# Kernel optimization log

Hardware: AMD Instinct MI355X
Metric: run time of the kernel (lower is better)

Reference implementation:

```python
import jax, jax.numpy as jnp
from jax import lax
import numpy as np

B, T, U, V = 4, 300, 64, 1024
FEAT, H, L = 80, 512, 3            # encoder: 3-layer bidirectional LSTM
HD = 512                           # decoder hidden (1 layer)
ENC_OUT = DEC_OUT = 512
INNER = 512
DMAX = max(FEAT, 2 * H)            # padded input dim for stacked encoder weights
NEG = -1e30


def setup_inputs() -> dict:
    key = jax.random.key(0)
    ks = jax.random.split(key, 20)
    s = 1.0 / np.sqrt(H)
    u = lambda k, shp: jax.random.uniform(k, shp, jnp.float32, -s, s)
    inputs = jax.random.normal(ks[0], (B, T, FEAT), jnp.float32)
    inputs_length = jax.random.randint(ks[1], (B,), T // 2, T + 1, jnp.int32)
    targets = jax.random.randint(ks[2], (B, U), 1, V, jnp.int32)
    targets_length = jax.random.randint(ks[3], (B,), U // 2, U + 1, jnp.int32)
    enc_Wih = u(ks[4], (L, 2, 4 * H, DMAX))   # layer0 uses first FEAT cols
    enc_Whh = u(ks[5], (L, 2, 4 * H, H))
    enc_b = u(ks[6], (L, 2, 4 * H))           # b_ih + b_hh fused
    enc_proj_W = u(ks[7], (ENC_OUT, 2 * H))
    enc_proj_b = u(ks[8], (ENC_OUT,))
    dec_emb = u(ks[9], (V, HD)).at[0].set(0.0)  # padding_idx=0
    dec_Wih = u(ks[10], (4 * HD, HD))
    dec_Whh = u(ks[11], (4 * HD, HD))
    dec_b = u(ks[12], (4 * HD,))
    dec_proj_W = u(ks[13], (DEC_OUT, HD))
    dec_proj_b = u(ks[14], (DEC_OUT,))
    j_fwd_W = u(ks[15], (INNER, ENC_OUT + DEC_OUT))
    j_fwd_b = u(ks[16], (INNER,))
    j_proj_W = u(ks[17], (V, INNER))
    j_proj_b = u(ks[18], (V,))
    return dict(inputs=inputs, inputs_length=inputs_length, targets=targets,
                targets_length=targets_length, enc_Wih=enc_Wih, enc_Whh=enc_Whh,
                enc_b=enc_b, enc_proj_W=enc_proj_W, enc_proj_b=enc_proj_b,
                dec_emb=dec_emb, dec_Wih=dec_Wih, dec_Whh=dec_Whh, dec_b=dec_b,
                dec_proj_W=dec_proj_W, dec_proj_b=dec_proj_b, j_fwd_W=j_fwd_W,
                j_fwd_b=j_fwd_b, j_proj_W=j_proj_W, j_proj_b=j_proj_b)


def lstm_layer(x, Wih, Whh, b):
    # x: [B, T, Din]; torch gate order (i, f, g, o)
    Bb = x.shape[0]
    Hh = Whh.shape[1]
    xg = jnp.einsum('btd,gd->btg', x, Wih) + b  # precompute input projections

    def step(carry, xt):
        h, c = carry
        g = xt + h @ Whh.T
        i, f, gg, o = jnp.split(g, 4, axis=-1)
        c = jax.nn.sigmoid(f) * c + jax.nn.sigmoid(i) * jnp.tanh(gg)
        h = jax.nn.sigmoid(o) * jnp.tanh(c)
        return (h, c), h

    z = jnp.zeros((Bb, Hh), x.dtype)
    _, hs = lax.scan(step, (z, z), xg.transpose(1, 0, 2))
    return hs.transpose(1, 0, 2)


def reverse_padded(x, lengths):
    # reverse each sequence within its valid length (packed-sequence semantics)
    t = jnp.arange(x.shape[1])
    idx = jnp.where(t[None] < lengths[:, None], lengths[:, None] - 1 - t[None], t[None])
    return jnp.take_along_axis(x, idx[:, :, None], axis=1)


def rnnt_loss(log_probs, targets, T_len, U_len):
    # log_probs: [B, T, U+1, V], blank = 0
    Bb, Tt, U1, _ = log_probs.shape
    Uu = U1 - 1
    blank = log_probs[..., 0]                                   # [B,T,U+1]
    idx = jnp.broadcast_to(targets[:, None, :, None], (Bb, Tt, Uu, 1))
    lab = jnp.take_along_axis(log_probs[:, :, :Uu, :], idx, axis=3)[..., 0]  # [B,T,U]

    def row_update(a, c):
        # solves x[u] = logaddexp(a[u], x[u-1] + c[u-1]) via log-space cumsum
        C = jnp.concatenate([jnp.zeros((Bb, 1), a.dtype), jnp.cumsum(c, axis=1)], axis=1)
        return C + lax.cumlogsumexp(a - C, axis=1)

    a0 = jnp.full((Bb, U1), NEG, log_probs.dtype).at[:, 0].set(0.0)
    alpha0 = row_update(a0, lab[:, 0])

    def step(alpha_prev, xs):
        bl_prev, lab_t = xs
        alpha = row_update(alpha_prev + bl_prev, lab_t)
        return alpha, alpha

    xs = (blank[:, :-1].transpose(1, 0, 2), lab[:, 1:].transpose(1, 0, 2))
    _, alphas = lax.scan(step, alpha0, xs)                      # [T-1,B,U+1]
    alphas = jnp.concatenate([alpha0[None], alphas], axis=0)    # [T,B,U+1]
    b_idx = jnp.arange(Bb)
    ll = alphas[T_len - 1, b_idx, U_len] + blank[b_idx, T_len - 1, U_len]
    return -jnp.mean(ll)


def reference(inputs, inputs_length, targets, targets_length, enc_Wih, enc_Whh,
              enc_b, enc_proj_W, enc_proj_b, dec_emb, dec_Wih, dec_Whh, dec_b,
              dec_proj_W, dec_proj_b, j_fwd_W, j_fwd_b, j_proj_W, j_proj_b):
    # ---- encoder: stacked bi-LSTM + projection ----
    mask = (jnp.arange(T)[None] < inputs_length[:, None])[..., None].astype(inputs.dtype)
    x = inputs
    for l in range(L):
        Din = x.shape[-1]
        fwd = lstm_layer(x, enc_Wih[l, 0, :, :Din], enc_Whh[l, 0], enc_b[l, 0])
        bwd = reverse_padded(
            lstm_layer(reverse_padded(x, inputs_length), enc_Wih[l, 1, :, :Din],
                       enc_Whh[l, 1], enc_b[l, 1]), inputs_length)
        x = jnp.concatenate([fwd, bwd], axis=-1) * mask
    enc = jnp.einsum('bth,oh->bto', x, enc_proj_W) + enc_proj_b  # [B,T,ENC_OUT]

    # ---- decoder: blank-prepended targets -> embed -> LSTM -> projection ----
    dec_in = jnp.pad(targets, ((0, 0), (1, 0)))                  # [B,U+1]
    demb = dec_emb[dec_in]
    dmask = (jnp.arange(U + 1)[None] < (targets_length + 1)[:, None])[..., None].astype(demb.dtype)
    dh = lstm_layer(demb, dec_Wih, dec_Whh, dec_b) * dmask
    dec = jnp.einsum('buh,oh->buo', dh, dec_proj_W) + dec_proj_b  # [B,U+1,DEC_OUT]

    # ---- joint: broadcast T x (U+1), split concat-matmul into two matmuls ----
    We, Wd = j_fwd_W[:, :ENC_OUT], j_fwd_W[:, ENC_OUT:]
    hj = jnp.tanh(jnp.einsum('bto,io->bti', enc, We)[:, :, None, :]
                  + jnp.einsum('buo,io->bui', dec, Wd)[:, None, :, :] + j_fwd_b)
    logits = jnp.einsum('btui,vi->btuv', hj, j_proj_W) + j_proj_b  # [B,T,U+1,V]
    log_probs = jax.nn.log_softmax(logits, axis=-1)

    return rnnt_loss(log_probs, targets, inputs_length, targets_length)
```

## Files before the change

### kernel.cpp

```cpp
#include <hip/hip_runtime.h>
#include <hip/hip_bf16.h>

#define B_ 4
#define T_ 300
#define U_ 64
#define U1_ 65
#define V_ 1024
#define H_ 512
#define G4_ 2048
#define NW_ 32
#define RPB_ (T_ * U1_)
#define NTILE_ 305
#define RPAD_ 19520

typedef __hip_bfloat16 bf16;
typedef unsigned long long u64;
typedef __attribute__((ext_vector_type(8))) short short8;
typedef __attribute__((ext_vector_type(4))) float floatx4;

__device__ __forceinline__ float b2f(bf16 x) { return __bfloat162float(x); }
__device__ __forceinline__ bf16 f2b(float x) { return __float2bfloat16(x); }
__device__ __forceinline__ short bf16bits(float x) {
  bf16 h = __float2bfloat16(x);
  return *reinterpret_cast<short*>(&h);
}
__device__ __forceinline__ short8 pack8(float4 a, float4 b) {
  short8 p;
  p[0] = bf16bits(a.x); p[1] = bf16bits(a.y); p[2] = bf16bits(a.z); p[3] = bf16bits(a.w);
  p[4] = bf16bits(b.x); p[5] = bf16bits(b.y); p[6] = bf16bits(b.z); p[7] = bf16bits(b.w);
  return p;
}
__device__ __forceinline__ float sigm_(float x) { return 1.f / (1.f + __expf(-x)); }
__device__ __forceinline__ float tanh_(float x) { return 1.f - 2.f / (1.f + __expf(2.f * x)); }
__device__ __forceinline__ float lae_(float x, float y) {
  float m = fmaxf(x, y);
  float n = fminf(x, y);
  return m + __logf(1.f + __expf(n - m));
}

__global__ void zero_hpk_kernel(u64* __restrict__ a) {
  int i = blockIdx.x * 256 + threadIdx.x;
  if (i < 7 * 4096) a[i] = 0ull;
}

__global__ void packw_kernel(const float* __restrict__ W, bf16* __restrict__ Wb, int n) {
  int i = blockIdx.x * 256 + threadIdx.x;
  if (i < n) Wb[i] = f2b(W[i]);
}

__global__ void prep_kernel(const float* __restrict__ in, bf16* __restrict__ x0) {
  int i = blockIdx.x * 256 + threadIdx.x;
  if (i < B_ * T_ * 128) {
    int k = i & 127;
    int row = i >> 7;
    float v = (k < 80) ? in[row * 80 + k] : 0.f;
    x0[(size_t)row * 1024 + k] = f2b(v);
  }
}

__global__ void embed_kernel(const float* __restrict__ emb, const int* __restrict__ tgt,
                             bf16* __restrict__ demb) {
  int i = blockIdx.x * 256 + threadIdx.x;
  if (i >= B_ * U1_ * 512) return;
  int k = i & 511;
  int bu = i >> 9;
  int u = bu % U1_, b = bu / U1_;
  int id = (u == 0) ? 0 : tgt[b * U_ + u - 1];
  demb[i] = f2b(emb[(size_t)id * 512 + k]);
}

__global__ __launch_bounds__(256) void gemm_kernel(
    const bf16* __restrict__ A, int lda,
    const float* __restrict__ W, int ldw,
    const float* __restrict__ bias,
    void* __restrict__ Cout, int out_f32, int ldc,
    int M, int K) {
  __shared__ __align__(16) bf16 As[64][72];
  __shared__ __align__(16) bf16 Bs[64][72];
  int m0 = blockIdx.x * 64, n0 = blockIdx.y * 64;
  int tid = threadIdx.x, w = tid >> 6, l = tid & 63;
  int l4 = l & 15, lq = l >> 4;
  floatx4 acc[4];
#pragma unroll
  for (int nt = 0; nt < 4; ++nt) acc[nt] = (floatx4){0.f, 0.f, 0.f, 0.f};
  for (int k0 = 0; k0 < K; k0 += 64) {
    __syncthreads();
#pragma unroll
    for (int q = 0; q < 2; ++q) {
      int cc = tid + q * 256;
      int r = cc >> 3, kc = (cc & 7) * 8;
      short8 va = {0, 0, 0, 0, 0, 0, 0, 0};
      int gm = m0 + r;
      if (gm < M) va = *(const short8*)(A + (size_t)gm * lda + k0 + kc);
      *(short8*)(&As[r][kc]) = va;
      const float* wp = W + (size_t)(n0 + r) * ldw + k0 + kc;
      float4 w0 = *(const float4*)(wp);
      float4 w1 = *(const float4*)(wp + 4);
      *(short8*)(&Bs[r][kc]) = pack8(w0, w1);
    }
    __syncthreads();
#pragma unroll
    for (int kk = 0; kk < 64; kk += 32) {
      short8 a = *(const short8*)(&As[w * 16 + l4][kk + lq * 8]);
#pragma unroll
      for (int nt = 0; nt < 4; ++nt) {
        short8 bb = *(const short8*)(&Bs[nt * 16 + l4][kk + lq * 8]);
        acc[nt] = __builtin_amdgcn_mfma_f32_16x16x32_bf16(a, bb, acc[nt], 0, 0, 0);
      }
    }
  }
#pragma unroll
  for (int nt = 0; nt < 4; ++nt) {
    int col = n0 + nt * 16 + l4;
    float bv = bias ? bias[col] : 0.f;
#pragma unroll
    for (int r = 0; r < 4; ++r) {
      int row = m0 + w * 16 + lq * 4 + r;
      if (row < M) {
        float v = acc[nt][r] + bv;
        if (out_f32) ((float*)Cout)[(size_t)row * ldc + col] = v;
        else ((bf16*)Cout)[(size_t)row * ldc + col] = f2b(v);
      }
    }
  }
}

__global__ __launch_bounds__(256, 1) void scan_kernel(
    const float* __restrict__ xg,
    const float* __restrict__ whh,
    const int* __restrict__ len_raw, int len_add,
    int Tmax, int bwd_mask,
    bf16* __restrict__ out, int out_stride,
    int dec_d,
    const float* __restrict__ xg2, const float* __restrict__ whh2,
    const int* __restrict__ len_raw2, int len_add2,
    int Tmax2, bf16* __restrict__ out2, int out_stride2,
    u64* __restrict__ hpk) {
  int w = blockIdx.x, d = blockIdx.y;
  int tid = threadIdx.x;
  bool isdec = (d == dec_d);
  const float* xg_d = isdec ? xg2 : xg + (size_t)d * B_ * Tmax * G4_;
  const float* whh_d = isdec ? whh2 : whh + (size_t)d * G4_ * H_;
  const int* lens = isdec ? len_raw2 : len_raw;
  int ladd = isdec ? len_add2 : len_add;
  int tmax = isdec ? Tmax2 : Tmax;
  bf16* outp = isdec ? out2 : out;
  int ostride = isdec ? out_stride2 : out_stride;
  int ocol = isdec ? 0 : d * H_;
  bool bwd = isdec ? false : ((bwd_mask >> d) & 1);
  u64* hp = hpk + (size_t)d * 4096;

  int sub = tid >> 6;
  int l = tid & 63;
  int col = l & 15;
  int lq = l >> 4;
  int gate = col & 3;
  int dloc = col >> 2;
  int dim = w * 16 + sub * 4 + dloc;
  int grow = gate * H_ + dim;
  int sb = l & 12;

  __shared__ int len_s[4];
  __shared__ __align__(16) bf16 h_lds[2][16][512];

  if (tid < 4) len_s[tid] = lens[tid] + ladd;
  {
    unsigned* hz = (unsigned*)&h_lds[0][0][0];
#pragma unroll
    for (int i = 0; i < 32; ++i) hz[tid + i * 256] = 0u;
  }

  short8 bfr[16];
  {
    const float* wp = whh_d + (size_t)grow * H_ + lq * 8;
#pragma unroll
    for (int ks2 = 0; ks2 < 16; ++ks2) {
      float4 w0 = *(const float4*)(wp + ks2 * 32);
      float4 w1 = *(const float4*)(wp + ks2 * 32 + 4);
      bfr[ks2] = pack8(w0, w1);
    }
  }
  __syncthreads();
  int smax = max(max(len_s[0], len_s[1]), max(len_s[2], len_s[3]));

  int D0 = sub * 128 + 2 * l;
  float cst = 0.f;
  char* hbase = (char*)&h_lds[0][0][0];
  unsigned rsw = (unsigned)((l & 7) << 4);
  unsigned rbyte = (unsigned)((l & 15) * 1024 + lq * 16);

  float xv[4];
  if (l < 16) {
#pragma unroll
    for (int b = 0; b < 4; ++b) {
      int lb = len_s[b];
      int rt = bwd ? (lb - 1) : 0;
      xv[b] = xg_d[((size_t)b * tmax + rt) * G4_ + grow];
    }
  }

  for (int s = 0; s < smax; ++s) {
    int p = s & 1;
    char* pl = hbase + p * 16384;
    if (s > 0) {
      const u64* src = hp + ((s - 1) & 1) * 2048;
      u64 v[8];
      for (;;) {
        bool ok = true;
#pragma unroll
        for (int b = 0; b < 4; ++b) {
          v[2 * b] = __hip_atomic_load(src + b * 512 + D0, __ATOMIC_RELAXED,
                                       __HIP_MEMORY_SCOPE_AGENT);
          v[2 * b + 1] = __hip_atomic_load(src + b * 512 + D0 + 1, __ATOMIC_RELAXED,
                                           __HIP_MEMORY_SCOPE_AGENT);
          ok &= ((int)(unsigned)v[2 * b] == s) & ((int)(unsigned)v[2 * b + 1] == s);
        }
        if (__all(ok)) break;
      }
      unsigned cb = (unsigned)(D0 * 2);
#pragma unroll
      for (int b = 0; b < 4; ++b) {
        float f0 = __uint_as_float((unsigned)(v[2 * b] >> 32));
        float f1 = __uint_as_float((unsigned)(v[2 * b + 1] >> 32));
        bf16 h0 = f2b(f0), h1 = f2b(f1);
        float r0 = f0 - b2f(h0), r1 = f1 - b2f(h1);
        bf16 e0 = f2b(r0), e1 = f2b(r1);
        unsigned hi = (unsigned)*(unsigned short*)&h0 |
                      ((unsigned)*(unsigned short*)&h1 << 16);
        unsigned lo = (unsigned)*(unsigned short*)&e0 |
                      ((unsigned)*(unsigned short*)&e1 << 16);
        *(unsigned*)(pl + (((unsigned)(b * 1024) + cb) ^ (unsigned)(b << 4))) = hi;
        *(unsigned*)(pl + (((unsigned)((b + 4) * 1024) + cb) ^ (unsigned)((b + 4) << 4))) = lo;
      }
    }
    __syncthreads();
    float xvn[4];
    if (l < 16) {
      int sn = s + 1;
#pragma unroll
      for (int b = 0; b < 4; ++b) {
        int lb = len_s[b];
        int rt = bwd ? (lb - 1 - sn) : sn;
        if (sn >= lb) rt = 0;
        xvn[b] = xg_d[((size_t)b * tmax + rt) * G4_ + grow];
      }
    }
    floatx4 accA = (floatx4){0.f, 0.f, 0.f, 0.f};
    floatx4 accB = (floatx4){0.f, 0.f, 0.f, 0.f};
#pragma unroll
    for (int k2 = 0; k2 < 16; k2 += 2) {
      short8 a0 = *(const short8*)(pl + ((rbyte + (unsigned)(k2 * 64)) ^ rsw));
      short8 a1 = *(const short8*)(pl + ((rbyte + (unsigned)((k2 + 1) * 64)) ^ rsw));
      accA = __builtin_amdgcn_mfma_f32_16x16x32_bf16(a0, bfr[k2], accA, 0, 0, 0);
      accB = __builtin_amdgcn_mfma_f32_16x16x32_bf16(a1, bfr[k2 + 1], accB, 0, 0, 0);
    }
    floatx4 acc = accA + accB;
    float hout = 0.f;
#pragma unroll
    for (int r = 0; r < 4; ++r) {
      float v2 = acc[r] + __shfl(acc[r], col + 16, 64);
      if (l < 16) v2 += xv[r];
      float gi = __shfl(v2, sb + 0, 64);
      float gf = __shfl(v2, sb + 1, 64);
      float gg = __shfl(v2, sb + 2, 64);
      float go = __shfl(v2, sb + 3, 64);
      if (l < 16 && (l & 3) == r && s < len_s[r]) {
        cst = sigm_(gf) * cst + sigm_(gi) * tanh_(gg);
        hout = sigm_(go) * tanh_(cst);
      }
    }
    if (l < 16) {
      int b = l & 3;
      u64 pkt = ((u64)__float_as_uint(hout) << 32) | (unsigned)(s + 1);
      __hip_atomic_store(hp + p * 2048 + b * 512 + dim, pkt,
                         __ATOMIC_RELAXED, __HIP_MEMORY_SCOPE_AGENT);
      if (s < len_s[b]) {
        int t = bwd ? (len_s[b] - 1 - s) : s;
        outp[((size_t)b * tmax + t) * ostride + ocol + dim] = f2b(hout);
      }
    }
#pragma unroll
    for (int b = 0; b < 4; ++b) xv[b] = xvn[b];
  }
}

__global__ __launch_bounds__(256) void joint_kernel(
    const float* __restrict__ ea, const float* __restrict__ da,
    const bf16* __restrict__ Wpb, const float* __restrict__ pb,
    const int* __restrict__ targets,
    float* __restrict__ blankraw, float* __restrict__ labraw,
    float* __restrict__ jstats) {
  __shared__ __align__(16) bf16 As[64][520];
  __shared__ __align__(16) bf16 Bs[256][72];
  __shared__ float bias_s[256];
  __shared__ int tgt_s[64];
  __shared__ float pstat[64][2][2];

  int tid = threadIdx.x;
  int tile = blockIdx.x, b = blockIdx.y;
  int r0 = tile * 64;

  if (tid < 64) {
    int r = r0 + tid;
    int u = r % U1_;
    tgt_s[tid] = (r < RPB_ && u < U_) ? targets[b * U_ + u] : -1;
  }
  int si = tid >> 2;
  int sseg = (tid & 3) * 16;
  int sr = r0 + si;
  bool svalid = sr < RPB_;
  int st = svalid ? sr / U1_ : 0;
  int su = svalid ? sr % U1_ : 0;
  const float* ep = ea + ((size_t)(b * T_ + st)) * 512 + sseg;
  const float* dp = da + ((size_t)(b * U1_ + su)) * 512 + sseg;

#pragma unroll
  for (int k0s = 0; k0s < 512; k0s += 64) {
    const float* e = ep + k0s;
    const float* d = dp + k0s;
#pragma unroll
    for (int h = 0; h < 2; ++h) {
      float4 e0 = *(const float4*)(e + h * 8);
      float4 e1 = *(const float4*)(e + h * 8 + 4);
      float4 d0 = *(const float4*)(d + h * 8);
      float4 d1 = *(const float4*)(d + h * 8 + 4);
      short8 pk = {0, 0, 0, 0, 0, 0, 0, 0};
      if (svalid) {
        pk[0] = bf16bits(tanh_(e0.x + d0.x));
        pk[1] = bf16bits(tanh_(e0.y + d0.y));
        pk[2] = bf16bits(tanh_(e0.z + d0.z));
        pk[3] = bf16bits(tanh_(e0.w + d0.w));
        pk[4] = bf16bits(tanh_(e1.x + d1.x));
        pk[5] = bf16bits(tanh_(e1.y + d1.y));
        pk[6] = bf16bits(tanh_(e1.z + d1.z));
        pk[7] = bf16bits(tanh_(e1.w + d1.w));
      }
      *(short8*)(&As[si][k0s + sseg + h * 8]) = pk;
    }
  }

  int wid = tid >> 6, l = tid & 63;
  int wm = wid >> 1, wn = wid & 1;
  int l4 = l & 15, lq = l >> 4;

  for (int cb = 0; cb < 4; ++cb) {
    bias_s[tid] = pb[cb * 256 + tid];

    floatx4 acc[2][8];
#pragma unroll
    for (int ms = 0; ms < 2; ++ms)
#pragma unroll
      for (int nt = 0; nt < 8; ++nt) acc[ms][nt] = (floatx4){0.f, 0.f, 0.f, 0.f};

    for (int k0 = 0; k0 < 512; k0 += 64) {
      __syncthreads();
#pragma unroll
      for (int q = 0; q < 8; ++q) {
        int cc = tid + q * 256;
        int r = cc >> 3, kc = (cc & 7) * 8;
        *(short8*)(&Bs[r][kc]) =
            *(const short8*)(Wpb + (size_t)(cb * 256 + r) * 512 + k0 + kc);
      }
      __syncthreads();
#pragma unroll
      for (int kk = 0; kk < 64; kk += 32) {
        short8 af[2], bf8[8];
#pragma unroll
        for (int ms = 0; ms < 2; ++ms)
          af[ms] = *(const short8*)(&As[wm * 32 + ms * 16 + l4][k0 + kk + lq * 8]);
#pragma unroll
        for (int nt = 0; nt < 8; ++nt)
          bf8[nt] = *(const short8*)(&Bs[wn * 128 + nt * 16 + l4][kk + lq * 8]);
#pragma unroll
        for (int ms = 0; ms < 2; ++ms)
#pragma unroll
          for (int nt = 0; nt < 8; ++nt)
            acc[ms][nt] = __builtin_amdgcn_mfma_f32_16x16x32_bf16(af[ms], bf8[nt], acc[ms][nt], 0, 0, 0);
      }
    }
#pragma unroll
    for (int ms = 0; ms < 2; ++ms) {
#pragma unroll
      for (int r = 0; r < 4; ++r) {
        int i = wm * 32 + ms * 16 + lq * 4 + r;
        int grow = r0 + i;
        bool valid = grow < RPB_;
        int tg = tgt_s[i];
        float v[8];
        float mx = -1e30f;
#pragma unroll
        for (int nt = 0; nt < 8; ++nt) {
          int colc = wn * 128 + nt * 16 + l4;
          float x = acc[ms][nt][r] + bias_s[colc];
          v[nt] = x;
          mx = fmaxf(mx, x);
          int gcol = cb * 256 + colc;
          if (valid) {
            if (gcol == 0) blankraw[(size_t)b * RPB_ + grow] = x;
            if (gcol == tg) labraw[(size_t)b * RPB_ + grow] = x;
          }
        }
#pragma unroll
        for (int dd = 1; dd < 16; dd <<= 1) mx = fmaxf(mx, __shfl_xor(mx, dd, 64));
        float se = 0.f;
#pragma unroll
        for (int nt = 0; nt < 8; ++nt) se += __expf(v[nt] - mx);
#pragma unroll
        for (int dd = 1; dd < 16; dd <<= 1) se += __shfl_xor(se, dd, 64);
        if (l4 == 0) { pstat[i][wn][0] = mx; pstat[i][wn][1] = se; }
      }
    }
    __syncthreads();
    if (tid < 64) {
      float ma = pstat[tid][0][0], sa = pstat[tid][0][1];
      float mb = pstat[tid][1][0], sb = pstat[tid][1][1];
      float mc = fmaxf(ma, mb);
      float sc = sa * __expf(ma - mc) + sb * __expf(mb - mc);
      size_t o = (((size_t)b * RPAD_ + r0 + tid) * 4 + cb) * 2;
      jstats[o] = mc;
      jstats[o + 1] = sc;
    }
  }
}

__global__ void finalize_kernel(const float* __restrict__ jstats,
                                float* __restrict__ blank, float* __restrict__ lab) {
  int g = blockIdx.x * 256 + threadIdx.x;
  if (g >= B_ * RPB_) return;
  int b = g / RPB_, r = g % RPB_;
  const float* st = jstats + ((size_t)b * RPAD_ + r) * 8;
  float M = fmaxf(fmaxf(st[0], st[2]), fmaxf(st[4], st[6]));
  float s = st[1] * __expf(st[0] - M) + st[3] * __expf(st[2] - M) +
            st[5] * __expf(st[4] - M) + st[7] * __expf(st[6] - M);
  float lse = M + __logf(s);
  blank[g] -= lse;
  if ((r % U1_) < U_) lab[g] -= lse;
}

__global__ void loss_kernel(const float* __restrict__ blank, const float* __restrict__ lab,
                            const int* __restrict__ Tl, const int* __restrict__ Ul,
                            float* __restrict__ outp) {
  int b = threadIdx.x >> 6;
  int l = threadIdx.x & 63;
  int TL = Tl[b], UL = Ul[b];
  float alpha_l = 0.f, alpha0 = 0.f;
  for (int t = 0; t < TL; ++t) {
    float a_u0, a_l1;
    if (t == 0) { a_u0 = 0.f; a_l1 = -1e30f; }
    else {
      const float* bl = blank + ((size_t)b * T_ + (t - 1)) * U1_;
      a_u0 = alpha0 + bl[0];
      a_l1 = alpha_l + bl[l + 1];
    }
    const float* lb = lab + ((size_t)b * T_ + t) * U1_;
    float C = lb[l];
#pragma unroll
    for (int dd = 1; dd < 64; dd <<= 1) {
      float o = __shfl_up(C, dd, 64);
      if (l >= dd) C += o;
    }
    float S = a_l1 - C;
#pragma unroll
    for (int dd = 1; dd < 64; dd <<= 1) {
      float o = __shfl_up(S, dd, 64);
      if (l >= dd) S = lae_(S, o);
    }
    alpha_l = C + lae_(a_u0, S);
    alpha0 = a_u0;
  }
  float av = (UL == 0) ? alpha0 : __shfl(alpha_l, UL - 1, 64);
  float ll = av + blank[((size_t)b * T_ + (TL - 1)) * U1_ + UL];
  __shared__ float lls[4];
  if (l == 0) lls[b] = ll;
  __syncthreads();
  if (threadIdx.x == 0) outp[0] = -0.25f * (lls[0] + lls[1] + lls[2] + lls[3]);
}

static constexpr size_t OFF_XG = 0;
static constexpr size_t OFF_XA = OFF_XG + (size_t)2 * B_ * T_ * G4_ * 4;
static constexpr size_t OFF_XB = OFF_XA + (size_t)B_ * T_ * 1024 * 2;
static constexpr size_t OFF_ENC = OFF_XB + (size_t)B_ * T_ * 1024 * 2;
static constexpr size_t OFF_EA = OFF_ENC + (size_t)B_ * T_ * 512 * 2;
static constexpr size_t OFF_DEMB = OFF_EA + (size_t)B_ * T_ * 512 * 4;
static constexpr size_t OFF_DXG = OFF_DEMB + (size_t)B_ * U1_ * 512 * 2;
static constexpr size_t OFF_DH = OFF_DXG + (size_t)B_ * U1_ * G4_ * 4;
static constexpr size_t OFF_DEC = OFF_DH + (size_t)B_ * U1_ * 512 * 2;
static constexpr size_t OFF_DA = OFF_DEC + (size_t)B_ * U1_ * 512 * 2;
static constexpr size_t OFF_BL = OFF_DA + (size_t)B_ * U1_ * 512 * 4;
static constexpr size_t OFF_LAB = OFF_BL + (size_t)B_ * T_ * U1_ * 4;
static constexpr size_t OFF_HPK = OFF_LAB + (size_t)B_ * T_ * U1_ * 4;
static constexpr size_t OFF_JST = OFF_HPK + (size_t)7 * 4096 * 8;
static constexpr size_t OFF_WPB = OFF_JST + (size_t)B_ * RPAD_ * 4 * 2 * 4;

extern "C" void kernel_launch(void* const* d_in, const int* in_sizes, int n_in,
                              void* d_out, int out_size, void* d_ws, size_t ws_size,
                              hipStream_t stream) {
  (void)in_sizes; (void)n_in; (void)out_size; (void)ws_size;
  const float* inputs = (const float*)d_in[0];
  const int* inputs_length = (const int*)d_in[1];
  const int* targets = (const int*)d_in[2];
  const int* targets_length = (const int*)d_in[3];
  const float* enc_Wih = (const float*)d_in[4];
  const float* enc_Whh = (const float*)d_in[5];
  const float* enc_b = (const float*)d_in[6];
  const float* enc_proj_W = (const float*)d_in[7];
  const float* enc_proj_b = (const float*)d_in[8];
  const float* dec_emb = (const float*)d_in[9];
  const float* dec_Wih = (const float*)d_in[10];
  const float* dec_Whh = (const float*)d_in[11];
  const float* dec_b = (const float*)d_in[12];
  const float* dec_proj_W = (const float*)d_in[13];
  const float* dec_proj_b = (const float*)d_in[14];
  const float* j_fwd_W = (const float*)d_in[15];
  const float* j_fwd_b = (const float*)d_in[16];
  const float* j_proj_W = (const float*)d_in[17];
  const float* j_proj_b = (const float*)d_in[18];

  char* ws = (char*)d_ws;
  float* xg = (float*)(ws + OFF_XG);
  bf16* xa = (bf16*)(ws + OFF_XA);
  bf16* xb = (bf16*)(ws + OFF_XB);
  bf16* encb = (bf16*)(ws + OFF_ENC);
  float* eab = (float*)(ws + OFF_EA);
  bf16* demb = (bf16*)(ws + OFF_DEMB);
  float* dxg = (float*)(ws + OFF_DXG);
  bf16* dh = (bf16*)(ws + OFF_DH);
  bf16* decb = (bf16*)(ws + OFF_DEC);
  float* dab = (float*)(ws + OFF_DA);
  float* blank = (float*)(ws + OFF_BL);
  float* lab = (float*)(ws + OFF_LAB);
  u64* hpk = (u64*)(ws + OFF_HPK);
  float* jstats = (float*)(ws + OFF_JST);
  bf16* wpb = (bf16*)(ws + OFF_WPB);

  zero_hpk_kernel<<<112, 256, 0, stream>>>(hpk);
  packw_kernel<<<2048, 256, 0, stream>>>(j_proj_W, wpb, V_ * 512);
  prep_kernel<<<600, 256, 0, stream>>>(inputs, xa);
  embed_kernel<<<520, 256, 0, stream>>>(dec_emb, targets, demb);

  gemm_kernel<<<dim3(5, 32), 256, 0, stream>>>(demb, 512, dec_Wih, 512, dec_b,
                                               dxg, 1, G4_, B_ * U1_, 512);
  for (int dd = 0; dd < 2; ++dd) {
    gemm_kernel<<<dim3(19, 32), 256, 0, stream>>>(
        xa, 1024, enc_Wih + (size_t)dd * G4_ * 1024, 1024, enc_b + (size_t)dd * G4_,
        xg + (size_t)dd * B_ * T_ * G4_, 1, G4_, B_ * T_, 128);
  }
  scan_kernel<<<dim3(NW_, 3), 256, 0, stream>>>(
      xg, enc_Whh, inputs_length, 0, T_, 2, xb, 1024,
      2, dxg, dec_Whh, targets_length, 1, U1_, dh, 512,
      hpk);

  gemm_kernel<<<dim3(5, 8), 256, 0, stream>>>(dh, 512, dec_proj_W, 512, dec_proj_b,
                                              decb, 0, 512, B_ * U1_, 512);
  gemm_kernel<<<dim3(5, 8), 256, 0, stream>>>(decb, 512, j_fwd_W + 512, 1024, j_fwd_b,
                                              dab, 1, 512, B_ * U1_, 512);

  bf16* xcur = xb;
  for (int lyr = 1; lyr < 3; ++lyr) {
    bf16* xnext = (xcur == xa) ? xb : xa;
    for (int dd = 0; dd < 2; ++dd) {
      gemm_kernel<<<dim3(19, 32), 256, 0, stream>>>(
          xcur, 1024,
          enc_Wih + (size_t)(lyr * 2 + dd) * G4_ * 1024, 1024,
          enc_b + (size_t)(lyr * 2 + dd) * G4_,
          xg + (size_t)dd * B_ * T_ * G4_, 1, G4_, B_ * T_, 1024);
    }
    scan_kernel<<<dim3(NW_, 2), 256, 0, stream>>>(
        xg, enc_Whh + (size_t)lyr * 2 * G4_ * H_,
        inputs_length, 0, T_, 2, xnext, 1024,
        -1, dxg, dec_Whh, targets_length, 1, U1_, dh, 512,
        hpk + (size_t)(3 + 2 * (lyr - 1)) * 4096);
    xcur = xnext;
  }
  gemm_kernel<<<dim3(19, 8), 256, 0, stream>>>(xcur, 1024, enc_proj_W, 1024, enc_proj_b,
                                               encb, 0, 512, B_ * T_, 1024);
  gemm_kernel<<<dim3(19, 8), 256, 0, stream>>>(encb, 512, j_fwd_W, 1024, (const float*)nullptr,
                                               eab, 1, 512, B_ * T_, 512);

  joint_kernel<<<dim3(NTILE_, B_), 256, 0, stream>>>(eab, dab, wpb, j_proj_b, targets,
                                                     blank, lab, jstats);
  finalize_kernel<<<(B_ * RPB_ + 255) / 256, 256, 0, stream>>>(jstats, blank, lab);
  loss_kernel<<<1, 256, 0, stream>>>(blank, lab, inputs_length, targets_length, (float*)d_out);
}
```

Measured before the change: 3.336 ms.

## Double-buffer joint weight tiles with register prefetch across flattened N/K loop

The joint GEMM's nested column-block and K loops become one flattened 32-iteration loop. Each iteration prefetches the next weight tile from global memory into registers, computes on the current LDS buffer, then writes the prefetch into the alternate LDS buffer. This cuts the barriers per K step from two to one and hides global load latency behind the MFMA work. Bias loads move into a single upfront copy. The cost is extra LDS for the second buffer and extra registers for the prefetch, which may reduce occupancy. A leftover no-op statement reassigns acc[ms][0] to itself.

New measurement: 3.383 ms. Within noise of the previous version (+1.4%).

```diff
diff --git a/kernel.cpp b/kernel.cpp
--- a/kernel.cpp
+++ b/kernel.cpp
@@ -291,8 +291,8 @@
     float* __restrict__ blankraw, float* __restrict__ labraw,
     float* __restrict__ jstats) {
   __shared__ __align__(16) bf16 As[64][520];
-  __shared__ __align__(16) bf16 Bs[256][72];
-  __shared__ float bias_s[256];
+  __shared__ __align__(16) bf16 Bs[2][256][72];
+  __shared__ float bias_s[4][256];
   __shared__ int tgt_s[64];
   __shared__ float pstat[64][2][2];
 
@@ -300,11 +300,27 @@
   int tile = blockIdx.x, b = blockIdx.y;
   int r0 = tile * 64;
 
+  int brow[8], bkc[8];
+#pragma unroll
+  for (int q = 0; q < 8; ++q) {
+    int cc = tid + q * 256;
+    brow[q] = cc >> 3;
+    bkc[q] = (cc & 7) * 8;
+  }
+
+  short8 breg[8];
+#pragma unroll
+  for (int q = 0; q < 8; ++q)
+    breg[q] = *(const short8*)(Wpb + (size_t)brow[q] * 512 + bkc[q]);
+
+#pragma unroll
+  for (int cbb = 0; cbb < 4; ++cbb) bias_s[cbb][tid] = pb[cbb * 256 + tid];
   if (tid < 64) {
     int r = r0 + tid;
     int u = r % U1_;
     tgt_s[tid] = (r < RPB_ && u < U_) ? targets[b * U_ + u] : -1;
   }
+
   int si = tid >> 2;
   int sseg = (tid & 3) * 16;
   int sr = r0 + si;
@@ -338,87 +354,103 @@
       *(short8*)(&As[si][k0s + sseg + h * 8]) = pk;
     }
   }
+#pragma unroll
+  for (int q = 0; q < 8; ++q) *(short8*)(&Bs[0][brow[q]][bkc[q]]) = breg[q];
+  __syncthreads();
 
   int wid = tid >> 6, l = tid & 63;
   int wm = wid >> 1, wn = wid & 1;
   int l4 = l & 15, lq = l >> 4;
 
-  for (int cb = 0; cb < 4; ++cb) {
-    bias_s[tid] = pb[cb * 256 + tid];
-
-    floatx4 acc[2][8];
-#pragma unroll
-    for (int ms = 0; ms < 2; ++ms)
-#pragma unroll
-      for (int nt = 0; nt < 8; ++nt) acc[ms][nt] = (floatx4){0.f, 0.f, 0.f, 0.f};
-
-    for (int k0 = 0; k0 < 512; k0 += 64) {
+  floatx4 acc[2][8];
+#pragma unroll
+  for (int ms = 0; ms < 2; ++ms)
+#pragma unroll
+    for (int nt = 0; nt < 8; ++nt) acc[ms][nt] = (floatx4){0.f, 0.f, 0.f, 0.f};
+
+#pragma unroll 1
+  for (int it = 0; it < 32; ++it) {
+    int cur = it & 1;
+    int cb = it >> 3;
+    int kloc = (it & 7) * 64;
+    int nxt = it + 1;
+    if (nxt < 32) {
+      int ncb = nxt >> 3;
+      int nkl = (nxt & 7) * 64;
+      const bf16* wb = Wpb + (size_t)(ncb * 256) * 512 + nkl;
+#pragma unroll
+      for (int q = 0; q < 8; ++q)
+        breg[q] = *(const short8*)(wb + (size_t)brow[q] * 512 + bkc[q]);
+    }
+#pragma unroll
+    for (int kk = 0; kk < 64; kk += 32) {
+      short8 af[2], bf8[8];
+#pragma unroll
+      for (int ms = 0; ms < 2; ++ms)
+        af[ms] = *(const short8*)(&As[wm * 32 + ms * 16 + l4][kloc + kk + lq * 8]);
+#pragma unroll
+      for (int nt = 0; nt < 8; ++nt)
+        bf8[nt] = *(const short8*)(&Bs[cur][wn * 128 + nt * 16 + l4][kk + lq * 8]);
+#pragma unroll
+      for (int ms = 0; ms < 2; ++ms)
+#pragma unroll
+        for (int nt = 0; nt < 8; ++nt)
+          acc[ms][nt] = __builtin_amdgcn_mfma_f32_16x16x32_bf16(af[ms], bf8[nt], acc[ms][nt], 0, 0, 0);
+    }
+    if (nxt < 32) {
+#pragma unroll
+      for (int q = 0; q < 8; ++q) *(short8*)(&Bs[nxt & 1][brow[q]][bkc[q]]) = breg[q];
+    }
+    __syncthreads();
+    if ((it & 7) == 7) {
+#pragma unroll
+      for (int ms = 0; ms < 2; ++ms) {
+#pragma unroll
+        for (int r = 0; r < 4; ++r) {
+          int i = wm * 32 + ms * 16 + lq * 4 + r;
+          int grow = r0 + i;
+          bool valid = grow < RPB_;
+          int tg = tgt_s[i];
+          float v[8];
+          float mx = -1e30f;
+#pragma unroll
+          for (int nt = 0; nt < 8; ++nt) {
+            int colc = wn * 128 + nt * 16 + l4;
+            float x = acc[ms][nt][r] + bias_s[cb][colc];
+            v[nt] = x;
+            mx = fmaxf(mx, x);
+            int gcol = cb * 256 + colc;
+            if (valid) {
+              if (gcol == 0) blankraw[(size_t)b * RPB_ + grow] = x;
+              if (gcol == tg) labraw[(size_t)b * RPB_ + grow] = x;
+            }
+          }
+#pragma unroll
+          for (int dd = 1; dd < 16; dd <<= 1) mx = fmaxf(mx, __shfl_xor(mx, dd, 64));
+          float se = 0.f;
+#pragma unroll
+          for (int nt = 0; nt < 8; ++nt) se += __expf(v[nt] - mx);
+#pragma unroll
+          for (int dd = 1; dd < 16; dd <<= 1) se += __shfl_xor(se, dd, 64);
+          if (l4 == 0) { pstat[i][wn][0] = mx; pstat[i][wn][1] = se; }
+          acc[ms][r * 2 & 0] = acc[ms][0];
+        }
+      }
       __syncthreads();
-#pragma unroll
-      for (int q = 0; q < 8; ++q) {
-        int cc = tid + q * 256;
-        int r = cc >> 3, kc = (cc & 7) * 8;
-        *(short8*)(&Bs[r][kc]) =
-            *(const short8*)(Wpb + (size_t)(cb * 256 + r) * 512 + k0 + kc);
-      }
+      if (tid < 64) {
+        float ma = pstat[tid][0][0], sa = pstat[tid][0][1];
+        float mb = pstat[tid][1][0], sb = pstat[tid][1][1];
+        float mc = fmaxf(ma, mb);
+        float sc = sa * __expf(ma - mc) + sb * __expf(mb - mc);
+        size_t o = (((size_t)b * RPAD_ + r0 + tid) * 4 + cb) * 2;
+        jstats[o] = mc;
+        jstats[o + 1] = sc;
+      }
+#pragma unroll
+      for (int ms = 0; ms < 2; ++ms)
+#pragma unroll
+        for (int nt = 0; nt < 8; ++nt) acc[ms][nt] = (floatx4){0.f, 0.f, 0.f, 0.f};
       __syncthreads();
-#pragma unroll
-      for (int kk = 0; kk < 64; kk += 32) {
-        short8 af[2], bf8[8];
-#pragma unroll
-        for (int ms = 0; ms < 2; ++ms)
-          af[ms] = *(const short8*)(&As[wm * 32 + ms * 16 + l4][k0 + kk + lq * 8]);
-#pragma unroll
-        for (int nt = 0; nt < 8; ++nt)
-          bf8[nt] = *(const short8*)(&Bs[wn * 128 + nt * 16 + l4][kk + lq * 8]);
-#pragma unroll
-        for (int ms = 0; ms < 2; ++ms)
-#pragma unroll
-          for (int nt = 0; nt < 8; ++nt)
-            acc[ms][nt] = __builtin_amdgcn_mfma_f32_16x16x32_bf16(af[ms], bf8[nt], acc[ms][nt], 0, 0, 0);
-      }
-    }
-#pragma unroll
-    for (int ms = 0; ms < 2; ++ms) {
-#pragma unroll
-      for (int r = 0; r < 4; ++r) {
-        int i = wm * 32 + ms * 16 + lq * 4 + r;
-        int grow = r0 + i;
-        bool valid = grow < RPB_;
-        int tg = tgt_s[i];
-        float v[8];
-        float mx = -1e30f;
-#pragma unroll
-        for (int nt = 0; nt < 8; ++nt) {
-          int colc = wn * 128 + nt * 16 + l4;
-          float x = acc[ms][nt][r] + bias_s[colc];
-          v[nt] = x;
-          mx = fmaxf(mx, x);
-          int gcol = cb * 256 + colc;
-          if (valid) {
-            if (gcol == 0) blankraw[(size_t)b * RPB_ + grow] = x;
-            if (gcol == tg) labraw[(size_t)b * RPB_ + grow] = x;
-          }
-        }
-#pragma unroll
-        for (int dd = 1; dd < 16; dd <<= 1) mx = fmaxf(mx, __shfl_xor(mx, dd, 64));
-        float se = 0.f;
-#pragma unroll
-        for (int nt = 0; nt < 8; ++nt) se += __expf(v[nt] - mx);
-#pragma unroll
-        for (int dd = 1; dd < 16; dd <<= 1) se += __shfl_xor(se, dd, 64);
-        if (l4 == 0) { pstat[i][wn][0] = mx; pstat[i][wn][1] = se; }
-      }
-    }
-    __syncthreads();
-    if (tid < 64) {
-      float ma = pstat[tid][0][0], sa = pstat[tid][0][1];
-      float mb = pstat[tid][1][0], sb = pstat[tid][1][1];
-      float mc = fmaxf(ma, mb);
-      float sc = sa * __expf(ma - mc) + sb * __expf(mb - mc);
-      size_t o = (((size_t)b * RPAD_ + r0 + tid) * 4 + cb) * 2;
-      jstats[o] = mc;
-      jstats[o + 1] = sc;
     }
   }
 }
```
